# Performance work log

Hardware: AMD Instinct MI355X
Metric: run time of the kernel (lower is better)

Reference implementation:

```python
import jax, jax.numpy as jnp
import numpy as np

V = 30        # vocab_size (amino-acid alphabet, identity embedding => one-hot)
T = 8192      # target_size (output vocab / conv out-channels)
K = 5         # filter_width
L = 512       # target_sequence_length == input seq len
B = 32        # batch


def setup_inputs() -> dict:
    key = jax.random.key(0)
    k1, k2, k3 = jax.random.split(key, 3)
    sentence_batch = jax.random.randint(k1, (B, L), 0, V)
    conv_w = jax.random.normal(k2, (T, V, K), jnp.float32) * (1.0 / np.sqrt(V * K))
    conv_b = jax.random.normal(k3, (T,), jnp.float32) * 0.01
    return {"sentence_batch": sentence_batch, "conv_w": conv_w, "conv_b": conv_b}


def reference(sentence_batch, conv_w, conv_b):
    # pad-or-slice to target_seq_length (here input len == L, so slice is a no-op)
    s = sentence_batch[:, :L]
    # frozen identity embedding == one-hot               [B, L, V]
    one_hot = jax.nn.one_hot(s, V, dtype=conv_w.dtype)
    x = jnp.transpose(one_hot, (0, 2, 1))                # [B, V, L]  (NCH)
    logits = jax.lax.conv_general_dilated(
        x, conv_w,
        window_strides=(1,),
        padding=[(K // 2, K // 2)],
        dimension_numbers=("NCH", "OIH", "NCH"),
    )                                                    # [B, T, L]
    logits = jnp.transpose(logits, (0, 2, 1)) + conv_b   # [B, L, T]
    # eval path: F.softmax over the target dim, then argmax
    probs = jax.nn.softmax(logits, axis=-1)
    new_seq = jnp.argmax(probs, axis=-1)                 # [B, L] int tokens
    return new_seq
```

## Files before the change

kernel.cpp:

```cpp
#include <hip/hip_runtime.h>

#define Vv 30
#define Tt 8192
#define Kk 5
#define Ll 512
#define Bb 32
#define NVK 150
#define ZROW 150
#define NROWS 151
#define TPOS (Bb * Ll)
#define PG 32
#define PPB (TPOS / PG)
#define PPT (PPB / 256)
#define TR 16
#define TW (Tt / TR)
#define TILE_T 64
#define NTILE (TW / TILE_T)
#define LSTRIDE 68

__global__ __launch_bounds__(256) void prep_w(
    const float* __restrict__ conv_w,
    const float* __restrict__ conv_b,
    float* __restrict__ wt)
{
    const int TILE = 32;
    __shared__ float tile[TILE * NVK];

    const int t0 = blockIdx.x * TILE;

    for (int i = threadIdx.x; i < TILE * NVK; i += 256)
        tile[i] = conv_w[t0 * NVK + i];
    __syncthreads();

    for (int i = threadIdx.x; i < NVK * TILE; i += 256) {
        const int vk = i >> 5;
        const int tl = i & 31;
        float v = tile[tl * NVK + vk];
        const int k = vk - (vk / Kk) * Kk;
        if (k == 2) v += conv_b[t0 + tl];
        wt[vk * Tt + t0 + tl] = v;
    }
    if (threadIdx.x < TILE)
        wt[ZROW * Tt + t0 + threadIdx.x] = 0.0f;
}

__global__ __launch_bounds__(256) void conv_argmax3(
    const int* __restrict__ seq,
    const float* __restrict__ wt,
    float2* __restrict__ partials)
{
    __shared__ float tile[NROWS * LSTRIDE];
    float4* __restrict__ tile4 = (float4*)tile;

    const int bid = blockIdx.x;
    const int pg  = bid & (PG - 1);
    const int tr  = bid >> 5;
    const int tid = threadIdx.x;

    int f4off[PPT][Kk];
#pragma unroll
    for (int j = 0; j < PPT; ++j) {
        const int pos = pg * PPB + j * 256 + tid;
        const int b = pos >> 9;
        const int l = pos & (Ll - 1);
#pragma unroll
        for (int k = 0; k < Kk; ++k) {
            const int lp = l + k - 2;
            const int row = (lp >= 0 && lp < Ll) ? (seq[b * Ll + lp] * Kk + k) : ZROW;
            f4off[j][k] = row * (LSTRIDE / 4);
        }
    }

    float bv[PPT];
    int   bt[PPT];
#pragma unroll
    for (int j = 0; j < PPT; ++j) { bv[j] = -1e30f; bt[j] = 0; }

    const int t_base = tr * TW;
    const float4* __restrict__ wsrc = (const float4*)wt;

    for (int tl = 0; tl < NTILE; ++tl) {
        const int t0 = t_base + tl * TILE_T;

        __syncthreads();
        for (int i = tid; i < NROWS * (TILE_T / 4); i += 256) {
            const int row = i >> 4;
            const int col = i & 15;
            tile4[row * (LSTRIDE / 4) + col] =
                wsrc[row * (Tt / 4) + (t0 >> 2) + col];
        }
        __syncthreads();

#pragma unroll 2
        for (int c4 = 0; c4 < TILE_T / 4; ++c4) {
            const int tg = t0 + c4 * 4;
#pragma unroll
            for (int j = 0; j < PPT; ++j) {
                const float4 a = tile4[f4off[j][0] + c4];
                const float4 c = tile4[f4off[j][1] + c4];
                const float4 d = tile4[f4off[j][2] + c4];
                const float4 e = tile4[f4off[j][3] + c4];
                const float4 f = tile4[f4off[j][4] + c4];
                const float s0 = ((a.x + c.x) + (d.x + e.x)) + f.x;
                const float s1 = ((a.y + c.y) + (d.y + e.y)) + f.y;
                const float s2 = ((a.z + c.z) + (d.z + e.z)) + f.z;
                const float s3 = ((a.w + c.w) + (d.w + e.w)) + f.w;
                if (s0 > bv[j]) { bv[j] = s0; bt[j] = tg; }
                if (s1 > bv[j]) { bv[j] = s1; bt[j] = tg + 1; }
                if (s2 > bv[j]) { bv[j] = s2; bt[j] = tg + 2; }
                if (s3 > bv[j]) { bv[j] = s3; bt[j] = tg + 3; }
            }
        }
    }

#pragma unroll
    for (int j = 0; j < PPT; ++j) {
        const int pos = pg * PPB + j * 256 + tid;
        partials[pos * TR + tr] = make_float2(bv[j], __int_as_float(bt[j]));
    }
}

__global__ __launch_bounds__(256) void combine(
    const float2* __restrict__ partials,
    int* __restrict__ out)
{
    const int pos = blockIdx.x * 256 + threadIdx.x;
    float bv = -1e30f;
    int   bt = 0;
#pragma unroll
    for (int tr = 0; tr < TR; ++tr) {
        const float2 p = partials[pos * TR + tr];
        const int t = __float_as_int(p.y);
        if (p.x > bv || (p.x == bv && t < bt)) { bv = p.x; bt = t; }
    }
    out[pos] = bt;
}

extern "C" void kernel_launch(void* const* d_in, const int* in_sizes, int n_in,
                              void* d_out, int out_size, void* d_ws, size_t ws_size,
                              hipStream_t stream)
{
    const int*   seq    = (const int*)d_in[0];
    const float* conv_w = (const float*)d_in[1];
    const float* conv_b = (const float*)d_in[2];
    int*         out    = (int*)d_out;
    float*       wt     = (float*)d_ws;
    float2*      part   = (float2*)((float*)d_ws + (size_t)NROWS * Tt);

    prep_w<<<Tt / 32, 256, 0, stream>>>(conv_w, conv_b, wt);
    conv_argmax3<<<PG * TR, 256, 0, stream>>>(seq, wt, part);
    combine<<<TPOS / 256, 256, 0, stream>>>(part, out);
}
```

Before: 129.5 us.

## Prune argmax search with per-chunk max upper bounds and a seeded lower bound

```diff
diff --git a/kernel.cpp b/kernel.cpp
--- a/kernel.cpp
+++ b/kernel.cpp
@@ -9,30 +9,43 @@
 #define ZROW 150
 #define NROWS 151
 #define TPOS (Bb * Ll)
+#define NC4 2048
+#define NC32 256
 #define PG 32
 #define PPB (TPOS / PG)
-#define PPT (PPB / 256)
-#define TR 16
-#define TW (Tt / TR)
-#define TILE_T 64
-#define NTILE (TW / TILE_T)
-#define LSTRIDE 68
+#define PPT 2
+#define TRm 16
+#define CPR (NC4 / TRm)
+#define TCH 64
+#define NTILE (CPR / TCH)
+#define LSG 17
+#define NPART 17
+
+__device__ inline float4 add4(float4 a, float4 b) {
+    return make_float4(a.x + b.x, a.y + b.y, a.z + b.z, a.w + b.w);
+}
+__device__ inline float4 tree5(float4 a, float4 b, float4 c, float4 d, float4 e) {
+    return add4(add4(add4(a, b), add4(c, d)), e);
+}
 
 __global__ __launch_bounds__(256) void prep_w(
     const float* __restrict__ conv_w,
     const float* __restrict__ conv_b,
-    float* __restrict__ wt)
-{
-    const int TILE = 32;
-    __shared__ float tile[TILE * NVK];
-
-    const int t0 = blockIdx.x * TILE;
-
-    for (int i = threadIdx.x; i < TILE * NVK; i += 256)
+    float* __restrict__ wt,
+    float* __restrict__ cm4,
+    float* __restrict__ cm32)
+{
+    __shared__ float tile[32 * NVK];
+    __shared__ float cml[NROWS * 8];
+
+    const int t0 = blockIdx.x * 32;
+    const int tid = threadIdx.x;
+
+    for (int i = tid; i < 32 * NVK; i += 256)
         tile[i] = conv_w[t0 * NVK + i];
     __syncthreads();
 
-    for (int i = threadIdx.x; i < NVK * TILE; i += 256) {
+    for (int i = tid; i < NVK * 32; i += 256) {
         const int vk = i >> 5;
         const int tl = i & 31;
         float v = tile[tl * NVK + vk];
@@ -40,24 +53,110 @@
         if (k == 2) v += conv_b[t0 + tl];
         wt[vk * Tt + t0 + tl] = v;
     }
-    if (threadIdx.x < TILE)
-        wt[ZROW * Tt + t0 + threadIdx.x] = 0.0f;
-}
-
-__global__ __launch_bounds__(256) void conv_argmax3(
+    if (tid < 32) wt[ZROW * Tt + t0 + tid] = 0.0f;
+
+    for (int idx = tid; idx < NROWS * 8; idx += 256) {
+        const int row = idx >> 3;
+        const int cj  = idx & 7;
+        float m;
+        if (row == ZROW) {
+            m = 0.0f;
+        } else {
+            const int k = row - (row / Kk) * Kk;
+            m = -1e30f;
+#pragma unroll
+            for (int q = 0; q < 4; ++q) {
+                const int tl = cj * 4 + q;
+                float v = tile[tl * NVK + row];
+                if (k == 2) v += conv_b[t0 + tl];
+                m = fmaxf(m, v);
+            }
+        }
+        cm4[row * NC4 + (t0 >> 2) + cj] = m;
+        cml[idx] = m;
+    }
+    __syncthreads();
+
+    for (int row = tid; row < NROWS; row += 256) {
+        float m = cml[row * 8];
+#pragma unroll
+        for (int q = 1; q < 8; ++q) m = fmaxf(m, cml[row * 8 + q]);
+        cm32[row * NC32 + blockIdx.x] = m;
+    }
+}
+
+__global__ __launch_bounds__(256) void seed_k(
     const int* __restrict__ seq,
     const float* __restrict__ wt,
+    const float* __restrict__ cm32,
+    float* __restrict__ lb,
     float2* __restrict__ partials)
 {
-    __shared__ float tile[NROWS * LSTRIDE];
-    float4* __restrict__ tile4 = (float4*)tile;
+    const int lane = threadIdx.x & 63;
+    const int pos  = blockIdx.x * 4 + (threadIdx.x >> 6);
+    const int b = pos >> 9;
+    const int l = pos & (Ll - 1);
+
+    int rows[Kk];
+#pragma unroll
+    for (int k = 0; k < Kk; ++k) {
+        const int lp = l + k - 2;
+        rows[k] = (lp >= 0 && lp < Ll) ? (seq[b * Ll + lp] * Kk + k) : ZROW;
+    }
+
+    const float4* __restrict__ c32_4 = (const float4*)cm32;
+    const float4 u = tree5(c32_4[rows[0] * 64 + lane], c32_4[rows[1] * 64 + lane],
+                           c32_4[rows[2] * 64 + lane], c32_4[rows[3] * 64 + lane],
+                           c32_4[rows[4] * 64 + lane]);
+    float mu = u.x; int mc = lane * 4;
+    if (u.y > mu) { mu = u.y; mc = lane * 4 + 1; }
+    if (u.z > mu) { mu = u.z; mc = lane * 4 + 2; }
+    if (u.w > mu) { mu = u.w; mc = lane * 4 + 3; }
+#pragma unroll
+    for (int m = 32; m >= 1; m >>= 1) {
+        const float om = __shfl_xor(mu, m);
+        const int   oc = __shfl_xor(mc, m);
+        if (om > mu || (om == mu && oc < mc)) { mu = om; mc = oc; }
+    }
+
+    const int t = mc * 32 + (lane & 31);
+    const float w0 = wt[rows[0] * Tt + t];
+    const float w1 = wt[rows[1] * Tt + t];
+    const float w2 = wt[rows[2] * Tt + t];
+    const float w3 = wt[rows[3] * Tt + t];
+    const float w4 = wt[rows[4] * Tt + t];
+    float bv = ((w0 + w1) + (w2 + w3)) + w4;
+    int   bt = t;
+#pragma unroll
+    for (int m = 32; m >= 1; m >>= 1) {
+        const float ov = __shfl_xor(bv, m);
+        const int   ot = __shfl_xor(bt, m);
+        if (ov > bv || (ov == bv && ot < bt)) { bv = ov; bt = ot; }
+    }
+
+    if (lane == 0) {
+        lb[pos] = bv;
+        partials[16 * TPOS + pos] = make_float2(bv, __int_as_float(bt));
+    }
+}
+
+__global__ __launch_bounds__(256) void conv_scan(
+    const int* __restrict__ seq,
+    const float* __restrict__ wt,
+    const float* __restrict__ cm4,
+    const float* __restrict__ lb,
+    float2* __restrict__ partials)
+{
+    __shared__ float4 tile4[NROWS * LSG];
 
     const int bid = blockIdx.x;
     const int pg  = bid & (PG - 1);
     const int tr  = bid >> 5;
     const int tid = threadIdx.x;
 
+    int rows[PPT][Kk];
     int f4off[PPT][Kk];
+    float lbv[PPT];
 #pragma unroll
     for (int j = 0; j < PPT; ++j) {
         const int pos = pg * PPB + j * 256 + tid;
@@ -67,8 +166,10 @@
         for (int k = 0; k < Kk; ++k) {
             const int lp = l + k - 2;
             const int row = (lp >= 0 && lp < Ll) ? (seq[b * Ll + lp] * Kk + k) : ZROW;
-            f4off[j][k] = row * (LSTRIDE / 4);
-        }
+            rows[j][k]  = row;
+            f4off[j][k] = row * LSG;
+        }
+        lbv[j] = lb[pos];
     }
 
     float bv[PPT];
@@ -76,39 +177,59 @@
 #pragma unroll
     for (int j = 0; j < PPT; ++j) { bv[j] = -1e30f; bt[j] = 0; }
 
-    const int t_base = tr * TW;
-    const float4* __restrict__ wsrc = (const float4*)wt;
+    const float4* __restrict__ cm4_4 = (const float4*)cm4;
+    const float4* __restrict__ wt4   = (const float4*)wt;
 
     for (int tl = 0; tl < NTILE; ++tl) {
-        const int t0 = t_base + tl * TILE_T;
+        const int cbase = tr * CPR + tl * TCH;
+        const int gbase = cbase >> 2;
 
         __syncthreads();
-        for (int i = tid; i < NROWS * (TILE_T / 4); i += 256) {
+        for (int i = tid; i < NROWS * 16; i += 256) {
             const int row = i >> 4;
             const int col = i & 15;
-            tile4[row * (LSTRIDE / 4) + col] =
-                wsrc[row * (Tt / 4) + (t0 >> 2) + col];
+            tile4[row * LSG + col] = cm4_4[row * 512 + gbase + col];
         }
         __syncthreads();
 
-#pragma unroll 2
-        for (int c4 = 0; c4 < TILE_T / 4; ++c4) {
-            const int tg = t0 + c4 * 4;
+        unsigned long long mask[PPT] = {0ull, 0ull};
+
+#pragma unroll 4
+        for (int g = 0; g < 16; ++g) {
 #pragma unroll
             for (int j = 0; j < PPT; ++j) {
-                const float4 a = tile4[f4off[j][0] + c4];
-                const float4 c = tile4[f4off[j][1] + c4];
-                const float4 d = tile4[f4off[j][2] + c4];
-                const float4 e = tile4[f4off[j][3] + c4];
-                const float4 f = tile4[f4off[j][4] + c4];
-                const float s0 = ((a.x + c.x) + (d.x + e.x)) + f.x;
-                const float s1 = ((a.y + c.y) + (d.y + e.y)) + f.y;
-                const float s2 = ((a.z + c.z) + (d.z + e.z)) + f.z;
-                const float s3 = ((a.w + c.w) + (d.w + e.w)) + f.w;
-                if (s0 > bv[j]) { bv[j] = s0; bt[j] = tg; }
-                if (s1 > bv[j]) { bv[j] = s1; bt[j] = tg + 1; }
-                if (s2 > bv[j]) { bv[j] = s2; bt[j] = tg + 2; }
-                if (s3 > bv[j]) { bv[j] = s3; bt[j] = tg + 3; }
+                const float4 u = tree5(tile4[f4off[j][0] + g], tile4[f4off[j][1] + g],
+                                       tile4[f4off[j][2] + g], tile4[f4off[j][3] + g],
+                                       tile4[f4off[j][4] + g]);
+                unsigned long long bits =
+                    (unsigned long long)((u.x >= lbv[j]) ? 1u : 0u)
+                  | ((unsigned long long)((u.y >= lbv[j]) ? 1u : 0u) << 1)
+                  | ((unsigned long long)((u.z >= lbv[j]) ? 1u : 0u) << 2)
+                  | ((unsigned long long)((u.w >= lbv[j]) ? 1u : 0u) << 3);
+                mask[j] |= bits << (g * 4);
+            }
+        }
+
+#pragma unroll
+        for (int j = 0; j < PPT; ++j) {
+            unsigned long long m = mask[j];
+            while (m) {
+                const int bidx = __ffsll(m) - 1;
+                m &= m - 1;
+                const int c = cbase + bidx;
+                const float4 e = tree5(wt4[rows[j][0] * 512 * 4 + c],
+                                       wt4[rows[j][1] * 512 * 4 + c],
+                                       wt4[rows[j][2] * 512 * 4 + c],
+                                       wt4[rows[j][3] * 512 * 4 + c],
+                                       wt4[rows[j][4] * 512 * 4 + c]);
+                int t = c * 4;
+                if (e.x > bv[j] || (e.x == bv[j] && t < bt[j])) { bv[j] = e.x; bt[j] = t; }
+                t = c * 4 + 1;
+                if (e.y > bv[j] || (e.y == bv[j] && t < bt[j])) { bv[j] = e.y; bt[j] = t; }
+                t = c * 4 + 2;
+                if (e.z > bv[j] || (e.z == bv[j] && t < bt[j])) { bv[j] = e.z; bt[j] = t; }
+                t = c * 4 + 3;
+                if (e.w > bv[j] || (e.w == bv[j] && t < bt[j])) { bv[j] = e.w; bt[j] = t; }
             }
         }
     }
@@ -116,7 +237,7 @@
 #pragma unroll
     for (int j = 0; j < PPT; ++j) {
         const int pos = pg * PPB + j * 256 + tid;
-        partials[pos * TR + tr] = make_float2(bv[j], __int_as_float(bt[j]));
+        partials[tr * TPOS + pos] = make_float2(bv[j], __int_as_float(bt[j]));
     }
 }
 
@@ -126,10 +247,10 @@
 {
     const int pos = blockIdx.x * 256 + threadIdx.x;
     float bv = -1e30f;
-    int   bt = 0;
-#pragma unroll
-    for (int tr = 0; tr < TR; ++tr) {
-        const float2 p = partials[pos * TR + tr];
+    int   bt = 0x7fffffff;
+#pragma unroll
+    for (int i = 0; i < NPART; ++i) {
+        const float2 p = partials[i * TPOS + pos];
         const int t = __float_as_int(p.y);
         if (p.x > bv || (p.x == bv && t < bt)) { bv = p.x; bt = t; }
     }
@@ -144,10 +265,15 @@
     const float* conv_w = (const float*)d_in[1];
     const float* conv_b = (const float*)d_in[2];
     int*         out    = (int*)d_out;
-    float*       wt     = (float*)d_ws;
-    float2*      part   = (float2*)((float*)d_ws + (size_t)NROWS * Tt);
-
-    prep_w<<<Tt / 32, 256, 0, stream>>>(conv_w, conv_b, wt);
-    conv_argmax3<<<PG * TR, 256, 0, stream>>>(seq, wt, part);
+
+    float* wt   = (float*)d_ws;
+    float* cm4  = wt  + (size_t)NROWS * Tt;
+    float* cm32 = cm4 + (size_t)NROWS * NC4;
+    float* lbp  = cm32 + (size_t)NROWS * NC32;
+    float2* part = (float2*)(lbp + TPOS);
+
+    prep_w<<<Tt / 32, 256, 0, stream>>>(conv_w, conv_b, wt, cm4, cm32);
+    seed_k<<<TPOS / 4, 256, 0, stream>>>(seq, wt, cm32, lbp, part);
+    conv_scan<<<PG * TRm, 256, 0, stream>>>(seq, wt, cm4, lbp, part);
     combine<<<TPOS / 256, 256, 0, stream>>>(part, out);
 }
```

Result: slower. 306.3 us (+136.5%).
